# Optimization experiments

Measured on AMD Instinct MI355X. Metric: run time of the kernel, lower is better.

Reference implementation:

```python
import jax, jax.numpy as jnp
import numpy as np

DIM = 512
HID = 1024        # dim * expansion_factor
QK = 128          # query_key_dim
G = 256           # group_size
EPS = 1e-5


def setup_inputs() -> dict:
    key = jax.random.key(0)
    ks = jax.random.split(key, 6)
    x = jax.random.normal(ks[0], (4, 4096, DIM), jnp.float32)
    ln_w = jnp.ones((DIM,), jnp.float32)
    ln_b = jnp.zeros((DIM,), jnp.float32)
    Wh = 0.02 * jax.random.normal(ks[1], (DIM, 2 * HID), jnp.float32)
    bh = jnp.zeros((2 * HID,), jnp.float32)
    Wqk = 0.02 * jax.random.normal(ks[2], (DIM, QK), jnp.float32)
    bqk = jnp.zeros((QK,), jnp.float32)
    gamma = 0.02 * jax.random.normal(ks[3], (4, QK), jnp.float32)  # nn.init.normal_(gamma, std=0.02)
    beta = jnp.zeros((4, QK), jnp.float32)
    Wo = 0.02 * jax.random.normal(ks[4], (HID, DIM), jnp.float32)
    bo = jnp.zeros((DIM,), jnp.float32)
    return {"x": x, "ln_w": ln_w, "ln_b": ln_b, "Wh": Wh, "bh": bh,
            "Wqk": Wqk, "bqk": bqk, "gamma": gamma, "beta": beta,
            "Wo": Wo, "bo": bo}


def reference(x, ln_w, ln_b, Wh, bh, Wqk, bqk, gamma, beta, Wo, bo):
    b, n, _ = x.shape
    g = n // G  # number of groups (n chosen as multiple of G -> no padding)

    # LayerNorm (torch uses biased variance)
    mu = jnp.mean(x, axis=-1, keepdims=True)
    var = jnp.mean((x - mu) ** 2, axis=-1, keepdims=True)
    normed = (x - mu) * jax.lax.rsqrt(var + EPS) * ln_w + ln_b

    # to_hidden: Linear -> SiLU, split into v / gate
    h = jax.nn.silu(normed @ Wh + bh)            # [b, n, 2*HID]
    v, gate = jnp.split(h, 2, axis=-1)           # each [b, n, HID]

    # to_qk: Linear -> SiLU, then 4-head offset/scale
    qk = jax.nn.silu(normed @ Wqk + bqk)         # [b, n, QK]
    qkh = qk[..., None, :] * gamma + beta        # [b, n, 4, QK]
    quad_q, lin_q, quad_k, lin_k = (qkh[..., i, :] for i in range(4))

    # group: b (g n) d -> b g n d
    grp = lambda t: t.reshape(b, g, G, t.shape[-1])
    qq, qk_, lq, lk, vv = map(grp, (quad_q, quad_k, lin_q, lin_k, v))

    # quadratic (group-local) attention with ReLU^2 scores, causal within group
    sim = jnp.einsum('bgid,bgjd->bgij', qq, qk_) / G
    attn = jnp.square(jnp.maximum(sim, 0.0))
    causal_mask = jnp.triu(jnp.ones((G, G), dtype=bool), 1)
    attn = jnp.where(causal_mask, 0.0, attn)
    quad_out = jnp.einsum('bgij,bgje->bgie', attn, vv)   # [b, g, G, HID]

    # linear attention across groups: per-group kv, exclusive cumsum over group dim
    lin_kv = jnp.einsum('bgnd,bgne->bgde', lk, vv) / G   # [b, g, QK, HID]
    lin_kv = jnp.cumsum(lin_kv, axis=1)
    lin_kv = jnp.pad(lin_kv, ((0, 0), (1, 0), (0, 0), (0, 0)))[:, :-1]
    lin_out = jnp.einsum('bgde,bgnd->bgne', lin_kv, lq)  # [b, g, G, HID]

    out = gate * (quad_out.reshape(b, n, HID) + lin_out.reshape(b, n, HID))
    return out @ Wo + bo + x
```

## Files before the change

kernel.cpp:

```cpp
#include <hip/hip_runtime.h>
#include <hip/hip_bf16.h>
#include <math.h>


#define BATCH 4
#define SEQ   4096
#define TROWS 16384
#define DIMD  512
#define HIDD  1024
#define QKD   128
#define GRP   256
#define NGRP  16
#define BGRP  64
#define EPIW  132
#define EPB   130

typedef unsigned short bfraw;
typedef __attribute__((ext_vector_type(8))) short bf16x8;
typedef __attribute__((ext_vector_type(8))) unsigned short u16x8;
typedef __attribute__((ext_vector_type(4))) unsigned int u32x4;
typedef __attribute__((ext_vector_type(4))) float f32x4;

__device__ __forceinline__ float bf2f(bfraw u) {
    union { float f; unsigned int i; } c;
    c.i = ((unsigned int)u) << 16;
    return c.f;
}
__device__ __forceinline__ bfraw f2bf(float f) {
    unsigned int x = __float_as_uint(f);
    unsigned int r = (x + 0x7fffu + ((x >> 16) & 1u)) >> 16;
    return (bfraw)r;
}
__device__ __forceinline__ unsigned int pkbf(float lo, float hi) {
    __hip_bfloat162 h2 = __float22bfloat162_rn(make_float2(lo, hi));
    union { __hip_bfloat162 h; unsigned int u; } c; c.h = h2;
    return c.u;
}
__device__ __forceinline__ void store16bf(bfraw* dst, const float* src) {
    u32x4 a, b;
    #pragma unroll
    for (int k = 0; k < 4; ++k) a[k] = pkbf(src[2 * k], src[2 * k + 1]);
    #pragma unroll
    for (int k = 0; k < 4; ++k) b[k] = pkbf(src[8 + 2 * k], src[8 + 2 * k + 1]);
    *(u32x4*)dst = a;
    *(u32x4*)(dst + 8) = b;
}
__device__ __forceinline__ float silu_f(float z) {
    return z / (1.f + __expf(-z));
}
__device__ __forceinline__ void gload_lds16(const void* g, void* l) {
    __builtin_amdgcn_global_load_lds(
        (const __attribute__((address_space(1))) unsigned int*)g,
        (__attribute__((address_space(3))) unsigned int*)l, 16, 0, 0);
}

__device__ __forceinline__ void mfma_step(const bfraw* As, const bfraw* Bs,
                                          f32x4 acc[4][4], int wm, int wn,
                                          int q, int mi) {
    bf16x8 af[4], bfg[4];
    #pragma unroll
    for (int i = 0; i < 4; ++i)
        af[i] = *(const bf16x8*)&As[(size_t)(wm * 64 + i * 16 + mi) * 32 + q * 8];
    #pragma unroll
    for (int j = 0; j < 4; ++j)
        bfg[j] = *(const bf16x8*)&Bs[(size_t)(wn * 64 + j * 16 + mi) * 32 + q * 8];
    #pragma unroll
    for (int i = 0; i < 4; ++i)
        #pragma unroll
        for (int j = 0; j < 4; ++j)
            acc[i][j] = __builtin_amdgcn_mfma_f32_16x16x32_bf16(af[i], bfg[j], acc[i][j], 0, 0, 0);
}

#define SMEMP_DECL                                              \
    __shared__ __align__(16) char smem_[33280];                 \
    bfraw* A0buf = (bfraw*)smem_;                               \
    bfraw* B0buf = (bfraw*)(smem_ + 8192);                      \
    bfraw* A1buf = (bfraw*)(smem_ + 16384);                     \
    bfraw* B1buf = (bfraw*)(smem_ + 24576);

#define PIPE_DSTS                                               \
    bfraw* a0d  = A0buf + wid * 512;                            \
    bfraw* a0d2 = A0buf + 2048 + wid * 512;                     \
    bfraw* b0d  = B0buf + wid * 512;                            \
    bfraw* b0d2 = B0buf + 2048 + wid * 512;                     \
    bfraw* a1d  = A1buf + wid * 512;                            \
    bfraw* a1d2 = A1buf + 2048 + wid * 512;                     \
    bfraw* b1d  = B1buf + wid * 512;                            \
    bfraw* b1d2 = B1buf + 2048 + wid * 512;

#define KLOOP_PRE(Abase, Astr, Bbase, Bstr)                                    \
    const bfraw* pa0 = (Abase) + (size_t)(t >> 2) * (Astr) + (t & 3) * 8;      \
    const bfraw* pa1 = pa0 + (size_t)64 * (Astr);                              \
    const bfraw* pb0 = (Bbase) + (size_t)(t >> 2) * (Bstr) + (t & 3) * 8;      \
    const bfraw* pb1 = pb0 + (size_t)64 * (Bstr);

#define STAGE0                                                                 \
    do { gload_lds16(pa0, a0d); gload_lds16(pa1, a0d2);                        \
         gload_lds16(pb0, b0d); gload_lds16(pb1, b0d2);                        \
         pa0 += 32; pa1 += 32; pb0 += 32; pb1 += 32; } while (0)
#define STAGE1                                                                 \
    do { gload_lds16(pa0, a1d); gload_lds16(pa1, a1d2);                        \
         gload_lds16(pb0, b1d); gload_lds16(pb1, b1d2);                        \
         pa0 += 32; pa1 += 32; pb0 += 32; pb1 += 32; } while (0)

#define PIPE_LOOP(NIT, Abase, Astr, Bbase, Bstr)                               \
    {                                                                          \
        KLOOP_PRE(Abase, Astr, Bbase, Bstr)                                    \
        STAGE0;                                                                \
        for (int it = 0; it < (NIT); it += 2) {                                \
            __syncthreads();                                                   \
            if (it + 1 < (NIT)) STAGE1;                                        \
            mfma_step(A0buf, B0buf, acc, wm, wn, q, mi);                       \
            __syncthreads();                                                   \
            if (it + 2 < (NIT)) STAGE0;                                        \
            if (it + 1 < (NIT))                                                \
                mfma_step(A1buf, B1buf, acc, wm, wn, q, mi);                   \
        }                                                                      \
        __syncthreads();                                                       \
    }

__device__ __forceinline__ int epi_row(int p, int lr) {
    return (lr < 16) ? (p * 16 + lr) : (64 + p * 16 + (lr - 16));
}

__global__ __launch_bounds__(256) void prep_kernel(const float* __restrict__ x,
                                                   const float* __restrict__ lnw,
                                                   const float* __restrict__ lnb,
                                                   const float* __restrict__ Wh,
                                                   const float* __restrict__ Wo,
                                                   const float* __restrict__ Wqk,
                                                   bfraw* __restrict__ normb,
                                                   bfraw* __restrict__ WhT,
                                                   bfraw* __restrict__ WoT,
                                                   bfraw* __restrict__ WqkT) {
    __shared__ float tile[32][33];
    int bid = blockIdx.x;
    int t = threadIdx.x;
    if (bid < 4096) {
        int row  = bid * 4 + (t >> 6);
        int lane = t & 63;
        const float* xr = x + (size_t)row * DIMD;
        float4 v0 = ((const float4*)xr)[lane];
        float4 v1 = ((const float4*)xr)[lane + 64];
        float s  = v0.x + v0.y + v0.z + v0.w + v1.x + v1.y + v1.z + v1.w;
        float ss = v0.x*v0.x + v0.y*v0.y + v0.z*v0.z + v0.w*v0.w
                 + v1.x*v1.x + v1.y*v1.y + v1.z*v1.z + v1.w*v1.w;
        #pragma unroll
        for (int off = 32; off; off >>= 1) {
            s  += __shfl_xor(s, off);
            ss += __shfl_xor(ss, off);
        }
        float mu  = s * (1.f / DIMD);
        float var = ss * (1.f / DIMD) - mu * mu;
        float inv = rsqrtf(var + 1e-5f);
        float4 w0 = ((const float4*)lnw)[lane],  w1 = ((const float4*)lnw)[lane + 64];
        float4 b0 = ((const float4*)lnb)[lane],  b1 = ((const float4*)lnb)[lane + 64];
        unsigned int o0 = pkbf((v0.x - mu) * inv * w0.x + b0.x,
                               (v0.y - mu) * inv * w0.y + b0.y);
        unsigned int o1 = pkbf((v0.z - mu) * inv * w0.z + b0.z,
                               (v0.w - mu) * inv * w0.w + b0.w);
        unsigned int o2 = pkbf((v1.x - mu) * inv * w1.x + b1.x,
                               (v1.y - mu) * inv * w1.y + b1.y);
        unsigned int o3 = pkbf((v1.z - mu) * inv * w1.z + b1.z,
                               (v1.w - mu) * inv * w1.w + b1.w);
        unsigned int* brow = (unsigned int*)(normb + (size_t)row * DIMD);
        ((uint2*)brow)[lane]      = make_uint2(o0, o1);
        ((uint2*)brow)[lane + 64] = make_uint2(o2, o3);
        return;
    }
    bid -= 4096;
    const float* in; bfraw* outp; int R, C, nx;
    if (bid < 1024)      { in = Wh;  outp = WhT;  R = DIMD; C = 2 * HIDD; nx = 64; }
    else if (bid < 1536) { bid -= 1024; in = Wo;  outp = WoT;  R = HIDD; C = DIMD; nx = 16; }
    else                 { bid -= 1536; in = Wqk; outp = WqkT; R = DIMD; C = QKD;  nx = 4; }
    int c0 = (bid % nx) * 32, r0 = (bid / nx) * 32;
    int tr = t >> 3, tc4 = (t & 7) * 4;
    float4 v = *(const float4*)&in[(size_t)(r0 + tr) * C + c0 + tc4];
    tile[tr][tc4 + 0] = v.x; tile[tr][tc4 + 1] = v.y;
    tile[tr][tc4 + 2] = v.z; tile[tr][tc4 + 3] = v.w;
    __syncthreads();
    ushort4 s;
    s.x = f2bf(tile[tc4 + 0][tr]);
    s.y = f2bf(tile[tc4 + 1][tr]);
    s.z = f2bf(tile[tc4 + 2][tr]);
    s.w = f2bf(tile[tc4 + 3][tr]);
    *(ushort4*)&outp[(size_t)(c0 + tr) * R + r0 + tc4] = s;
}

__global__ __launch_bounds__(1024, 4) void gemm_h256(
    const bfraw* __restrict__ A,
    const bfraw* __restrict__ WhT,
    const bfraw* __restrict__ WqkT,
    const float* __restrict__ bh,
    const float* __restrict__ bqk,
    const float* __restrict__ gamma,
    const float* __restrict__ beta,
    bfraw* __restrict__ vT,
    bfraw* __restrict__ gate,
    bfraw* __restrict__ qq,
    bfraw* __restrict__ lq,
    bfraw* __restrict__ kk,
    bfraw* __restrict__ lkT) {
    __shared__ __align__(16) char smem_[131072];
    const int t = threadIdx.x;
    const int lane = t & 63, wid = t >> 6;
    const int wm = wid >> 2, wn = wid & 3;
    const int q = lane >> 4, mi = lane & 15;
    int nid = (blockIdx.x & 7) * 72 + (blockIdx.x >> 3);
    const int ct = nid % 9, by = nid / 9;
    const int r0 = by * 256, c0 = ct * 256;

    const int lslot = (t & 7) ^ ((t >> 3) & 7);
    const int srow  = 2 * (t >> 3) + (lslot >> 2);
    const int skel  = (lslot & 3) * 8;
    const bfraw* Asrc = A + (size_t)(r0 + srow) * DIMD + skel;
    const bfraw* Bsrc;
    if (ct < 8) {
        Bsrc = WhT + (size_t)(c0 + srow) * DIMD + skel;
    } else {
        Bsrc = WqkT + (size_t)(srow & 127) * DIMD + skel;
    }
    const int swz = ((((mi & 1) << 2) | q) ^ ((mi >> 1) & 7)) << 4;
    const int a_off = (wm * 32 + (mi >> 1)) * 128 + swz;
    const int b_off = (wn * 32 + (mi >> 1)) * 128 + swz;

#define GH_STAGE(KT, SLOT)                                                    \
    do {                                                                      \
        char* sb_ = smem_ + (SLOT) * 32768;                                   \
        gload_lds16(Asrc + (KT) * 32, sb_ + t * 16);                          \
        gload_lds16(Bsrc + (KT) * 32, sb_ + 16384 + t * 16);                  \
    } while (0)

    f32x4 acc[4][4] = {};
    GH_STAGE(0, 0);
    GH_STAGE(1, 1);
    GH_STAGE(2, 2);
    asm volatile("s_waitcnt vmcnt(4)" ::: "memory");
    __builtin_amdgcn_s_barrier();

    #pragma unroll
    for (int j = 0; j < 16; ++j) {
        const char* cb = smem_ + (j & 3) * 32768;
        bf16x8 af[4], bfr[4];
        #pragma unroll
        for (int mf = 0; mf < 4; ++mf)
            af[mf] = *(const bf16x8*)(cb + a_off + mf * 1024);
        #pragma unroll
        for (int nf = 0; nf < 4; ++nf)
            bfr[nf] = *(const bf16x8*)(cb + 16384 + b_off + nf * 1024);
        if (j + 3 < 16) GH_STAGE(j + 3, (j + 3) & 3);
        __builtin_amdgcn_s_setprio(1);
        #pragma unroll
        for (int mf = 0; mf < 4; ++mf)
            #pragma unroll
            for (int nf = 0; nf < 4; ++nf)
                acc[mf][nf] = __builtin_amdgcn_mfma_f32_16x16x32_bf16(
                    af[mf], bfr[nf], acc[mf][nf], 0, 0, 0);
        __builtin_amdgcn_s_setprio(0);
        if (j + 3 < 16)      asm volatile("s_waitcnt vmcnt(4)" ::: "memory");
        else if (j + 2 < 16) asm volatile("s_waitcnt vmcnt(2)" ::: "memory");
        else if (j + 1 < 16) asm volatile("s_waitcnt vmcnt(0)" ::: "memory");
        __builtin_amdgcn_s_barrier();
    }
#undef GH_STAGE

    float* epi = (float*)smem_;
    if (ct == 8) {
        float* gbl = (float*)(smem_ + 67584);
        if (t < 512) { gbl[t] = gamma[t]; gbl[t + 512] = beta[t]; }
        float bq4[4];
        #pragma unroll
        for (int nf = 0; nf < 4; ++nf)
            bq4[nf] = (wn < 2) ? bqk[wn * 64 + nf * 16 + mi] : 0.f;
        #pragma unroll
        for (int p = 0; p < 4; ++p) {
            if (wm == p && wn < 2) {
                #pragma unroll
                for (int mf = 0; mf < 4; ++mf)
                    #pragma unroll
                    for (int nf = 0; nf < 4; ++nf)
                        #pragma unroll
                        for (int rg = 0; rg < 4; ++rg)
                            epi[(mf * 16 + q * 4 + rg) * 132 + wn * 64 + nf * 16 + mi] =
                                silu_f(acc[mf][nf][rg] + bq4[nf]);
            }
            __syncthreads();
            if (t < 512) {
                int lr = t >> 3, cs = (t & 7) * 16;
                float z[16];
                #pragma unroll
                for (int k = 0; k < 16; ++k) z[k] = epi[lr * 132 + cs + k];
                size_t growr = (size_t)(r0 + p * 64 + lr) * QKD + cs;
                #pragma unroll
                for (int hd = 0; hd < 3; ++hd) {
                    bfraw* arr = (hd == 0) ? qq : (hd == 1) ? lq : kk;
                    float tmp[16];
                    #pragma unroll
                    for (int k = 0; k < 16; ++k)
                        tmp[k] = z[k] * gbl[hd * 128 + cs + k] + gbl[512 + hd * 128 + cs + k];
                    store16bf(arr + growr, tmp);
                }
            } else {
                int tt = t - 512;
                int c = tt >> 2, jh = (tt & 3) * 16;
                float g3 = gbl[384 + c], e3 = gbl[896 + c];
                float tmp[16];
                #pragma unroll
                for (int k = 0; k < 16; ++k)
                    tmp[k] = epi[(jh + k) * 132 + c] * g3 + e3;
                store16bf(lkT + ((size_t)by * QKD + c) * GRP + p * 64 + jh, tmp);
            }
            __syncthreads();
        }
        return;
    }
    float bias4[4];
    #pragma unroll
    for (int nf = 0; nf < 4; ++nf)
        bias4[nf] = bh[c0 + wn * 64 + nf * 16 + mi];
    if (ct < 4) {
        #pragma unroll
        for (int p = 0; p < 4; ++p) {
            if (wm == p) {
                #pragma unroll
                for (int mf = 0; mf < 4; ++mf)
                    #pragma unroll
                    for (int nf = 0; nf < 4; ++nf)
                        #pragma unroll
                        for (int rg = 0; rg < 4; ++rg)
                            epi[(mf * 16 + q * 4 + rg) * 257 + wn * 64 + nf * 16 + mi] =
                                silu_f(acc[mf][nf][rg] + bias4[nf]);
            }
            __syncthreads();
            int e2 = t >> 2, js = (t & 3) * 16;
            float tmp[16];
            #pragma unroll
            for (int k = 0; k < 16; ++k)
                tmp[k] = epi[(js + k) * 257 + e2];
            store16bf(vT + ((size_t)by * HIDD + c0 + e2) * GRP + p * 64 + js, tmp);
            __syncthreads();
        }
    } else {
        #pragma unroll
        for (int p = 0; p < 4; ++p) {
            if (wm == p) {
                #pragma unroll
                for (int mf = 0; mf < 4; ++mf)
                    #pragma unroll
                    for (int nf = 0; nf < 4; ++nf)
                        #pragma unroll
                        for (int rg = 0; rg < 4; ++rg)
                            epi[(mf * 16 + q * 4 + rg) * 260 + wn * 64 + nf * 16 + mi] =
                                silu_f(acc[mf][nf][rg] + bias4[nf]);
            }
            __syncthreads();
            int lr = t >> 4, cs = (t & 15) * 16;
            float tmp[16];
            #pragma unroll
            for (int k = 0; k < 16; ++k)
                tmp[k] = epi[lr * 260 + cs + k];
            store16bf(gate + (size_t)(r0 + p * 64 + lr) * HIDD + (c0 - HIDD) + cs, tmp);
            __syncthreads();
        }
    }
}

__global__ __launch_bounds__(256) void simkv_kernel(const bfraw* __restrict__ qq,
                                                    const bfraw* __restrict__ kk,
                                                    bfraw* __restrict__ attn,
                                                    const bfraw* __restrict__ vT,
                                                    const bfraw* __restrict__ lkT,
                                                    bfraw* __restrict__ kvT_raw) {
    SMEMP_DECL
    float* epi = (float*)smem_;
    int t = threadIdx.x;
    int lane = t & 63, wid = t >> 6;
    int wm = wid >> 1, wn = wid & 1;
    int q = lane >> 4, mi = lane & 15;
    int bid = blockIdx.x;
    f32x4 acc[4][4] = {};
    PIPE_DSTS
    if (bid < 512) {
        int bg = bid >> 3;
        int row0 = (bid & 7) * 128;
        PIPE_LOOP(8, vT + (size_t)bg * HIDD * GRP + (size_t)row0 * GRP, GRP,
                  lkT + (size_t)bg * QKD * GRP, GRP)
        bfraw* outg = kvT_raw + (size_t)bg * HIDD * QKD;
        #pragma unroll
        for (int p = 0; p < 4; ++p) {
            #pragma unroll
            for (int j = 0; j < 4; ++j)
                #pragma unroll
                for (int rg = 0; rg < 4; ++rg)
                    epi[(wm * 16 + q * 4 + rg) * EPIW + wn * 64 + j * 16 + mi] = acc[p][j][rg];
            __syncthreads();
            int lr = t >> 3, c0t = (t & 7) * 16;
            int gr = row0 + epi_row(p, lr);
            store16bf(outg + (size_t)gr * QKD + c0t, &epi[lr * EPIW + c0t]);
            __syncthreads();
        }
        return;
    }
    int i = bid - 512;
    int bg = i & 63;
    int tid = i >> 6;
    int ry = (tid == 0) ? 0 : 1;
    int rx = (tid == 2) ? 1 : 0;
    int row0 = ry * 128, col0 = rx * 128;
    PIPE_LOOP(4, qq + (size_t)(bg * GRP + row0) * QKD, QKD,
              kk + (size_t)(bg * GRP + col0) * QKD, QKD)
    bfraw* ag = attn + (size_t)bg * GRP * GRP;
    #pragma unroll
    for (int p = 0; p < 4; ++p) {
        #pragma unroll
        for (int j = 0; j < 4; ++j) {
            int colg = col0 + wn * 64 + j * 16 + mi;
            #pragma unroll
            for (int rg = 0; rg < 4; ++rg) {
                int rowg = row0 + wm * 64 + p * 16 + q * 4 + rg;
                float s = acc[p][j][rg] * (1.f / GRP);
                s = fmaxf(s, 0.f);
                s = s * s;
                epi[(wm * 16 + q * 4 + rg) * EPIW + wn * 64 + j * 16 + mi] =
                    (colg > rowg) ? 0.f : s;
            }
        }
        __syncthreads();
        int lr = t >> 3, c0t = (t & 7) * 16;
        int gr = row0 + epi_row(p, lr);
        store16bf(ag + (size_t)gr * GRP + col0 + c0t, &epi[lr * EPIW + c0t]);
        __syncthreads();
    }
}

__global__ __launch_bounds__(256) void cumsum2_kernel(const bfraw* __restrict__ raw,
                                                      bfraw* __restrict__ ex) {
    int idx = blockIdx.x * 256 + threadIdx.x;
    int b = idx >> 17;
    int r = idx & 131071;
    const bfraw* rp = raw + (size_t)b * NGRP * 131072 + r;
    bfraw* ep = ex + (size_t)b * NGRP * 131072 + r;
    float run = 0.f;
    #pragma unroll
    for (int g = 0; g < NGRP; ++g) {
        ep[(size_t)g * 131072] = f2bf(run);
        run += bf2f(rp[(size_t)g * 131072]) * (1.f / GRP);
    }
}

__global__ __launch_bounds__(256) void quadlin_mfma(const bfraw* __restrict__ attn,
                                                    const bfraw* __restrict__ vT,
                                                    const bfraw* __restrict__ lq,
                                                    const bfraw* __restrict__ kvT_ex,
                                                    const bfraw* __restrict__ gate,
                                                    bfraw* __restrict__ gated) {
    int bg = blockIdx.z;
    int row0 = blockIdx.y * 128;
    int col0 = blockIdx.x * 128;
    SMEMP_DECL
    float* epi = (float*)smem_;
    int t = threadIdx.x;
    int lane = t & 63, wid = t >> 6;
    int wm = wid >> 1, wn = wid & 1;
    int q = lane >> 4, mi = lane & 15;
    f32x4 acc[4][4] = {};
    PIPE_DSTS
    {
        int nit = (row0 + 128) >> 5;
        PIPE_LOOP(nit, attn + (size_t)bg * GRP * GRP + (size_t)row0 * GRP, GRP,
                  vT + (size_t)bg * HIDD * GRP + (size_t)col0 * GRP, GRP)
    }
    PIPE_LOOP(4, lq + (size_t)(bg * GRP + row0) * QKD, QKD,
              kvT_ex + (size_t)bg * HIDD * QKD + (size_t)col0 * QKD, QKD)
    #pragma unroll
    for (int p = 0; p < 4; ++p) {
        #pragma unroll
        for (int j = 0; j < 4; ++j)
            #pragma unroll
            for (int rg = 0; rg < 4; ++rg)
                epi[(wm * 16 + q * 4 + rg) * EPIW + wn * 64 + j * 16 + mi] = acc[p][j][rg];
        __syncthreads();
        int lr = t >> 3, c0t = (t & 7) * 16;
        int gr = row0 + epi_row(p, lr);
        size_t grow = (size_t)bg * GRP + gr;
        const float* src = &epi[lr * EPIW + c0t];
        const bfraw* gsrc = gate + grow * HIDD + col0 + c0t;
        u16x8 g0 = *(const u16x8*)gsrc;
        u16x8 g1 = *(const u16x8*)(gsrc + 8);
        float tmp[16];
        #pragma unroll
        for (int k = 0; k < 8; ++k) tmp[k] = src[k] * bf2f(g0[k]);
        #pragma unroll
        for (int k = 0; k < 8; ++k) tmp[8 + k] = src[8 + k] * bf2f(g1[k]);
        store16bf(gated + grow * HIDD + col0 + c0t, tmp);
        __syncthreads();
    }
}

__global__ __launch_bounds__(1024, 4) void gemm_final(
    const bfraw* __restrict__ A,
    const bfraw* __restrict__ BT,
    const float* __restrict__ bo,
    const float* __restrict__ x,
    float* __restrict__ out) {
    __shared__ __align__(16) char smem_[147456];
    const int t = threadIdx.x;
    const int lane = t & 63, wid = t >> 6;
    const int wm = wid >> 2, wn = wid & 3;
    const int q = lane >> 4, mi = lane & 15;
    int nid = (blockIdx.x & 7) * 32 + (blockIdx.x >> 3);
    const int by = nid >> 2, cx = nid & 3;
    const int r0 = by * 256, c0 = cx * 128;

    const int lslot = (t & 7) ^ ((t >> 3) & 7);
    const int a_row = 2 * (t >> 3) + (lslot >> 2);
    const int a_kel = (lslot & 3) * 8;
    const bfraw* Asrc = A + (size_t)(r0 + a_row) * HIDD + a_kel;
    const int u = t & 511;
    const int lsb = (u & 7) ^ ((u >> 3) & 7);
    const int b_row = 2 * (u >> 3) + (lsb >> 2);
    const int b_kel = (lsb & 3) * 8 + (t >> 9) * 32;
    const bfraw* Bsrc = BT + (size_t)(c0 + b_row) * HIDD + b_kel;

    const int swz = ((((mi & 1) << 2) | q) ^ ((mi >> 1) & 7)) << 4;
    const int a_off = (wm * 32 + (mi >> 1)) * 128 + swz;
    const int b_off = (wn * 16 + (mi >> 1)) * 128 + swz;

#define GF_STAGE(SS, SLOT)                                                    \
    do {                                                                      \
        char* sb_ = smem_ + (SLOT) * 49152;                                   \
        gload_lds16(Asrc + (SS) * 64,      sb_ + t * 16);                     \
        gload_lds16(Asrc + (SS) * 64 + 32, sb_ + 16384 + t * 16);             \
        gload_lds16(Bsrc + (SS) * 64,      sb_ + 32768 + t * 16);             \
    } while (0)

    f32x4 acc[4][2] = {};
    GF_STAGE(0, 0);
    GF_STAGE(1, 1);
    asm volatile("s_waitcnt vmcnt(3)" ::: "memory");
    __builtin_amdgcn_s_barrier();

    #pragma unroll
    for (int ss = 0; ss < 16; ++ss) {
        if (ss + 2 < 16) GF_STAGE(ss + 2, (ss + 2) % 3);
        const char* cb = smem_ + (ss % 3) * 49152;
        #pragma unroll
        for (int h = 0; h < 2; ++h) {
            bf16x8 af[4], bfr[2];
            #pragma unroll
            for (int mf = 0; mf < 4; ++mf)
                af[mf] = *(const bf16x8*)(cb + h * 16384 + a_off + mf * 1024);
            #pragma unroll
            for (int nf = 0; nf < 2; ++nf)
                bfr[nf] = *(const bf16x8*)(cb + 32768 + h * 8192 + b_off + nf * 1024);
            __builtin_amdgcn_s_setprio(1);
            #pragma unroll
            for (int mf = 0; mf < 4; ++mf)
                #pragma unroll
                for (int nf = 0; nf < 2; ++nf)
                    acc[mf][nf] = __builtin_amdgcn_mfma_f32_16x16x32_bf16(
                        af[mf], bfr[nf], acc[mf][nf], 0, 0, 0);
            __builtin_amdgcn_s_setprio(0);
        }
        if (ss + 2 < 16)      asm volatile("s_waitcnt vmcnt(3)" ::: "memory");
        else if (ss + 1 < 16) asm volatile("s_waitcnt vmcnt(0)" ::: "memory");
        __builtin_amdgcn_s_barrier();
    }
#undef GF_STAGE

    float* epi = (float*)smem_;
    float bo2[2];
    #pragma unroll
    for (int nf = 0; nf < 2; ++nf)
        bo2[nf] = bo[c0 + wn * 32 + nf * 16 + mi];
    #pragma unroll
    for (int p = 0; p < 4; ++p) {
        if (wm == p) {
            #pragma unroll
            for (int mf = 0; mf < 4; ++mf)
                #pragma unroll
                for (int nf = 0; nf < 2; ++nf)
                    #pragma unroll
                    for (int rg = 0; rg < 4; ++rg)
                        epi[(mf * 16 + q * 4 + rg) * 132 + wn * 32 + nf * 16 + mi] =
                            acc[mf][nf][rg] + bo2[nf];
        }
        __syncthreads();
        int lr = t >> 4, cs = (t & 15) * 8;
        const float* src = epi + lr * 132 + cs;
        const float* xs = x + (size_t)(r0 + p * 64 + lr) * DIMD + c0 + cs;
        float* dst = out + (size_t)(r0 + p * 64 + lr) * DIMD + c0 + cs;
        #pragma unroll
        for (int v = 0; v < 2; ++v) {
            float4 a = ((const float4*)src)[v];
            float4 xv = ((const float4*)xs)[v];
            a.x += xv.x; a.y += xv.y; a.z += xv.z; a.w += xv.w;
            ((float4*)dst)[v] = a;
        }
        __syncthreads();
    }
}

extern "C" void kernel_launch(void* const* d_in, const int* in_sizes, int n_in,
                              void* d_out, int out_size, void* d_ws, size_t ws_size,
                              hipStream_t stream) {
    const float* x     = (const float*)d_in[0];
    const float* ln_w  = (const float*)d_in[1];
    const float* ln_b  = (const float*)d_in[2];
    const float* Wh    = (const float*)d_in[3];
    const float* bh    = (const float*)d_in[4];
    const float* Wqk   = (const float*)d_in[5];
    const float* bqk   = (const float*)d_in[6];
    const float* gamma = (const float*)d_in[7];
    const float* beta  = (const float*)d_in[8];
    const float* Wo    = (const float*)d_in[9];
    const float* bo    = (const float*)d_in[10];
    float* out = (float*)d_out;

    char* outb_ = (char*)d_out;
    bfraw* attn = (bfraw*)(outb_);
    bfraw* qq   = (bfraw*)(outb_ + 8388608);
    bfraw* kk   = (bfraw*)(outb_ + 12582912);
    bfraw* lq   = (bfraw*)(outb_ + 16777216);
    bfraw* WhT  = (bfraw*)(outb_ + 20971520);
    bfraw* WqkT = (bfraw*)(outb_ + 23068672);

    char* wsb = (char*)d_ws;
    bfraw* vT      = (bfraw*)(wsb);
    bfraw* gate    = (bfraw*)(wsb + 33554432);
    bfraw* gated   = (bfraw*)(wsb + 67108864);
    bfraw* normb   = (bfraw*)(wsb + 100663296);
    bfraw* kvT_raw = (bfraw*)(wsb + 117440512);
    bfraw* kvT_ex  = (bfraw*)(wsb + 134217728);
    bfraw* lkT     = (bfraw*)(wsb + 150994944);
    bfraw* WoT     = (bfraw*)(wsb + 155189248);

    prep_kernel<<<4096 + 1024 + 512 + 64, 256, 0, stream>>>(
        x, ln_w, ln_b, Wh, Wo, Wqk, normb, WhT, WoT, WqkT);
    gemm_h256<<<576, 1024, 0, stream>>>(
        normb, WhT, WqkT, bh, bqk, gamma, beta, vT, gate, qq, lq, kk, lkT);
    simkv_kernel<<<512 + 192, 256, 0, stream>>>(qq, kk, attn, vT, lkT, kvT_raw);
    cumsum2_kernel<<<(BATCH * QKD * HIDD) / 256, 256, 0, stream>>>(kvT_raw, kvT_ex);
    quadlin_mfma<<<dim3(HIDD / 128, GRP / 128, BGRP), 256, 0, stream>>>(
        attn, vT, lq, kvT_ex, gate, gated);
    gemm_final<<<256, 1024, 0, stream>>>(gated, WoT, bo, x, out);
}
```

Before: 270.2 us.

## Shrink hidden GEMM tile to 128x256 with 512 threads and triple buffering

The first projection GEMM now uses 128-row tiles with 512-thread blocks instead of 256x256 tiles with 1024 threads, so twice as many blocks are launched. The LDS pipeline drops from four stages to three, each 24 KB, cutting shared memory per block from 128 KB to 72 KB. The epilogues are reindexed so vT, lkT and the q/k heads are written at half-group offsets. The aim is more resident blocks per CU and better load balance across the grid, at the cost of less operand reuse per block and more B-matrix traffic.

```diff
diff --git a/kernel.cpp b/kernel.cpp
--- a/kernel.cpp
+++ b/kernel.cpp
@@ -44,6 +44,12 @@
     for (int k = 0; k < 4; ++k) b[k] = pkbf(src[8 + 2 * k], src[8 + 2 * k + 1]);
     *(u32x4*)dst = a;
     *(u32x4*)(dst + 8) = b;
+}
+__device__ __forceinline__ void store8bf(bfraw* dst, const float* src) {
+    u32x4 a;
+    #pragma unroll
+    for (int k = 0; k < 4; ++k) a[k] = pkbf(src[2 * k], src[2 * k + 1]);
+    *(u32x4*)dst = a;
 }
 __device__ __forceinline__ float silu_f(float z) {
     return z / (1.f + __expf(-z));
@@ -187,7 +193,7 @@
     *(ushort4*)&outp[(size_t)(c0 + tr) * R + r0 + tc4] = s;
 }
 
-__global__ __launch_bounds__(1024, 4) void gemm_h256(
+__global__ __launch_bounds__(512, 4) void gemm_h256(
     const bfraw* __restrict__ A,
     const bfraw* __restrict__ WhT,
     const bfraw* __restrict__ WqkT,
@@ -201,24 +207,29 @@
     bfraw* __restrict__ lq,
     bfraw* __restrict__ kk,
     bfraw* __restrict__ lkT) {
-    __shared__ __align__(16) char smem_[131072];
+    __shared__ __align__(16) char smem_[73728];
     const int t = threadIdx.x;
     const int lane = t & 63, wid = t >> 6;
     const int wm = wid >> 2, wn = wid & 3;
     const int q = lane >> 4, mi = lane & 15;
-    int nid = (blockIdx.x & 7) * 72 + (blockIdx.x >> 3);
+    int nid = (blockIdx.x & 7) * 144 + (blockIdx.x >> 3);
     const int ct = nid % 9, by = nid / 9;
-    const int r0 = by * 256, c0 = ct * 256;
+    const int r0 = by * 128, c0 = ct * 256;
+    const int bg = r0 >> 8;
+    const int jb0 = r0 & 255;
 
     const int lslot = (t & 7) ^ ((t >> 3) & 7);
     const int srow  = 2 * (t >> 3) + (lslot >> 2);
     const int skel  = (lslot & 3) * 8;
     const bfraw* Asrc = A + (size_t)(r0 + srow) * DIMD + skel;
-    const bfraw* Bsrc;
+    const bfraw* Bsrc0;
+    const bfraw* Bsrc1;
     if (ct < 8) {
-        Bsrc = WhT + (size_t)(c0 + srow) * DIMD + skel;
+        Bsrc0 = WhT + (size_t)(c0 + srow) * DIMD + skel;
+        Bsrc1 = Bsrc0 + (size_t)128 * DIMD;
     } else {
-        Bsrc = WqkT + (size_t)(srow & 127) * DIMD + skel;
+        Bsrc0 = WqkT + (size_t)srow * DIMD + skel;
+        Bsrc1 = Bsrc0;
     }
     const int swz = ((((mi & 1) << 2) | q) ^ ((mi >> 1) & 7)) << 4;
     const int a_off = (wm * 32 + (mi >> 1)) * 128 + swz;
@@ -226,29 +237,29 @@
 
 #define GH_STAGE(KT, SLOT)                                                    \
     do {                                                                      \
-        char* sb_ = smem_ + (SLOT) * 32768;                                   \
-        gload_lds16(Asrc + (KT) * 32, sb_ + t * 16);                          \
-        gload_lds16(Bsrc + (KT) * 32, sb_ + 16384 + t * 16);                  \
+        char* sb_ = smem_ + (SLOT) * 24576;                                   \
+        gload_lds16(Asrc  + (KT) * 32, sb_ + t * 16);                         \
+        gload_lds16(Bsrc0 + (KT) * 32, sb_ + 8192 + t * 16);                  \
+        gload_lds16(Bsrc1 + (KT) * 32, sb_ + 16384 + t * 16);                 \
     } while (0)
 
     f32x4 acc[4][4] = {};
     GH_STAGE(0, 0);
     GH_STAGE(1, 1);
-    GH_STAGE(2, 2);
-    asm volatile("s_waitcnt vmcnt(4)" ::: "memory");
+    asm volatile("s_waitcnt vmcnt(3)" ::: "memory");
     __builtin_amdgcn_s_barrier();
 
     #pragma unroll
     for (int j = 0; j < 16; ++j) {
-        const char* cb = smem_ + (j & 3) * 32768;
+        if (j + 2 < 16) GH_STAGE(j + 2, (j + 2) % 3);
+        const char* cb = smem_ + (j % 3) * 24576;
         bf16x8 af[4], bfr[4];
         #pragma unroll
         for (int mf = 0; mf < 4; ++mf)
             af[mf] = *(const bf16x8*)(cb + a_off + mf * 1024);
         #pragma unroll
         for (int nf = 0; nf < 4; ++nf)
-            bfr[nf] = *(const bf16x8*)(cb + 16384 + b_off + nf * 1024);
-        if (j + 3 < 16) GH_STAGE(j + 3, (j + 3) & 3);
+            bfr[nf] = *(const bf16x8*)(cb + 8192 + b_off + nf * 1024);
         __builtin_amdgcn_s_setprio(1);
         #pragma unroll
         for (int mf = 0; mf < 4; ++mf)
@@ -257,8 +268,7 @@
                 acc[mf][nf] = __builtin_amdgcn_mfma_f32_16x16x32_bf16(
                     af[mf], bfr[nf], acc[mf][nf], 0, 0, 0);
         __builtin_amdgcn_s_setprio(0);
-        if (j + 3 < 16)      asm volatile("s_waitcnt vmcnt(4)" ::: "memory");
-        else if (j + 2 < 16) asm volatile("s_waitcnt vmcnt(2)" ::: "memory");
+        if (j + 2 < 16)      asm volatile("s_waitcnt vmcnt(3)" ::: "memory");
         else if (j + 1 < 16) asm volatile("s_waitcnt vmcnt(0)" ::: "memory");
         __builtin_amdgcn_s_barrier();
     }
@@ -266,49 +276,52 @@
 
     float* epi = (float*)smem_;
     if (ct == 8) {
-        float* gbl = (float*)(smem_ + 67584);
-        if (t < 512) { gbl[t] = gamma[t]; gbl[t + 512] = beta[t]; }
+        float* gbl = (float*)(smem_ + 36864);
+        gbl[t] = gamma[t];
+        gbl[t + 512] = beta[t];
         float bq4[4];
         #pragma unroll
         for (int nf = 0; nf < 4; ++nf)
             bq4[nf] = (wn < 2) ? bqk[wn * 64 + nf * 16 + mi] : 0.f;
         #pragma unroll
-        for (int p = 0; p < 4; ++p) {
-            if (wm == p && wn < 2) {
-                #pragma unroll
-                for (int mf = 0; mf < 4; ++mf)
+        for (int p2 = 0; p2 < 4; ++p2) {
+            if (wm == (p2 >> 1) && wn < 2) {
+                #pragma unroll
+                for (int mf2 = 0; mf2 < 2; ++mf2) {
+                    int mf = ((p2 & 1) << 1) + mf2;
                     #pragma unroll
                     for (int nf = 0; nf < 4; ++nf)
                         #pragma unroll
                         for (int rg = 0; rg < 4; ++rg)
-                            epi[(mf * 16 + q * 4 + rg) * 132 + wn * 64 + nf * 16 + mi] =
+                            epi[(mf2 * 16 + q * 4 + rg) * 132 + wn * 64 + nf * 16 + mi] =
                                 silu_f(acc[mf][nf][rg] + bq4[nf]);
+                }
             }
             __syncthreads();
-            if (t < 512) {
-                int lr = t >> 3, cs = (t & 7) * 16;
-                float z[16];
-                #pragma unroll
-                for (int k = 0; k < 16; ++k) z[k] = epi[lr * 132 + cs + k];
-                size_t growr = (size_t)(r0 + p * 64 + lr) * QKD + cs;
+            {
+                int lr = t >> 4, cs = (t & 15) * 8;
+                float z[8];
+                #pragma unroll
+                for (int k = 0; k < 8; ++k) z[k] = epi[lr * 132 + cs + k];
+                size_t growr = (size_t)(r0 + p2 * 32 + lr) * QKD + cs;
                 #pragma unroll
                 for (int hd = 0; hd < 3; ++hd) {
                     bfraw* arr = (hd == 0) ? qq : (hd == 1) ? lq : kk;
-                    float tmp[16];
+                    float tmp[8];
                     #pragma unroll
-                    for (int k = 0; k < 16; ++k)
+                    for (int k = 0; k < 8; ++k)
                         tmp[k] = z[k] * gbl[hd * 128 + cs + k] + gbl[512 + hd * 128 + cs + k];
-                    store16bf(arr + growr, tmp);
+                    store8bf(arr + growr, tmp);
                 }
-            } else {
-                int tt = t - 512;
-                int c = tt >> 2, jh = (tt & 3) * 16;
+            }
+            {
+                int c = t >> 2, jh = (t & 3) * 8;
                 float g3 = gbl[384 + c], e3 = gbl[896 + c];
-                float tmp[16];
-                #pragma unroll
-                for (int k = 0; k < 16; ++k)
+                float tmp[8];
+                #pragma unroll
+                for (int k = 0; k < 8; ++k)
                     tmp[k] = epi[(jh + k) * 132 + c] * g3 + e3;
-                store16bf(lkT + ((size_t)by * QKD + c) * GRP + p * 64 + jh, tmp);
+                store8bf(lkT + ((size_t)bg * QKD + c) * GRP + jb0 + p2 * 32 + jh, tmp);
             }
             __syncthreads();
         }
@@ -320,38 +333,42 @@
         bias4[nf] = bh[c0 + wn * 64 + nf * 16 + mi];
     if (ct < 4) {
         #pragma unroll
-        for (int p = 0; p < 4; ++p) {
-            if (wm == p) {
-                #pragma unroll
-                for (int mf = 0; mf < 4; ++mf)
+        for (int p2 = 0; p2 < 4; ++p2) {
+            if (wm == (p2 >> 1)) {
+                #pragma unroll
+                for (int mf2 = 0; mf2 < 2; ++mf2) {
+                    int mf = ((p2 & 1) << 1) + mf2;
                     #pragma unroll
                     for (int nf = 0; nf < 4; ++nf)
                         #pragma unroll
                         for (int rg = 0; rg < 4; ++rg)
-                            epi[(mf * 16 + q * 4 + rg) * 257 + wn * 64 + nf * 16 + mi] =
+                            epi[(mf2 * 16 + q * 4 + rg) * 257 + wn * 64 + nf * 16 + mi] =
                                 silu_f(acc[mf][nf][rg] + bias4[nf]);
+                }
             }
             __syncthreads();
-            int e2 = t >> 2, js = (t & 3) * 16;
+            int e2 = t >> 1, js = (t & 1) * 16;
             float tmp[16];
             #pragma unroll
             for (int k = 0; k < 16; ++k)
                 tmp[k] = epi[(js + k) * 257 + e2];
-            store16bf(vT + ((size_t)by * HIDD + c0 + e2) * GRP + p * 64 + js, tmp);
+            store16bf(vT + ((size_t)bg * HIDD + c0 + e2) * GRP + jb0 + p2 * 32 + js, tmp);
             __syncthreads();
         }
     } else {
         #pragma unroll
-        for (int p = 0; p < 4; ++p) {
-            if (wm == p) {
-                #pragma unroll
-                for (int mf = 0; mf < 4; ++mf)
+        for (int p2 = 0; p2 < 4; ++p2) {
+            if (wm == (p2 >> 1)) {
+                #pragma unroll
+                for (int mf2 = 0; mf2 < 2; ++mf2) {
+                    int mf = ((p2 & 1) << 1) + mf2;
                     #pragma unroll
                     for (int nf = 0; nf < 4; ++nf)
                         #pragma unroll
                         for (int rg = 0; rg < 4; ++rg)
-                            epi[(mf * 16 + q * 4 + rg) * 260 + wn * 64 + nf * 16 + mi] =
+                            epi[(mf2 * 16 + q * 4 + rg) * 260 + wn * 64 + nf * 16 + mi] =
                                 silu_f(acc[mf][nf][rg] + bias4[nf]);
+                }
             }
             __syncthreads();
             int lr = t >> 4, cs = (t & 15) * 16;
@@ -359,7 +376,7 @@
             #pragma unroll
             for (int k = 0; k < 16; ++k)
                 tmp[k] = epi[lr * 260 + cs + k];
-            store16bf(gate + (size_t)(r0 + p * 64 + lr) * HIDD + (c0 - HIDD) + cs, tmp);
+            store16bf(gate + (size_t)(r0 + p2 * 32 + lr) * HIDD + (c0 - HIDD) + cs, tmp);
             __syncthreads();
         }
     }
@@ -637,7 +654,7 @@
 
     prep_kernel<<<4096 + 1024 + 512 + 64, 256, 0, stream>>>(
         x, ln_w, ln_b, Wh, Wo, Wqk, normb, WhT, WoT, WqkT);
-    gemm_h256<<<576, 1024, 0, stream>>>(
+    gemm_h256<<<1152, 512, 0, stream>>>(
         normb, WhT, WqkT, bh, bqk, gamma, beta, vT, gate, qq, lq, kk, lkT);
     simkv_kernel<<<512 + 192, 256, 0, stream>>>(qq, kk, attn, vT, lkT, kvT_raw);
     cumsum2_kernel<<<(BATCH * QKD * HIDD) / 256, 256, 0, stream>>>(kvT_raw, kvT_ex);
```

Result: faster. 257.7 us (-4.6%).
